# Kernel optimization log

Hardware: AMD Instinct MI355X
Metric: run time of the kernel (lower is better)

Reference implementation:

```python
import jax, jax.numpy as jnp
import numpy as np

HEADS = 8
DIM_HEAD = 160
QUERY_DIM = 1280
INNER = HEADS * DIM_HEAD  # 1280
B, S = 2, 4096


def setup_inputs() -> dict:
    key = jax.random.key(0)
    ks = jax.random.split(key, 7)
    scale = 0.02
    return {
        "hidden_states": jax.random.normal(ks[0], (B, QUERY_DIM, 1, S), jnp.float32),
        "context": jax.random.normal(ks[1], (B, QUERY_DIM, 1, S), jnp.float32),
        "mask": jnp.zeros((B, S, 1, 1), jnp.float32),
        "Wq": jax.random.normal(ks[2], (INNER, QUERY_DIM), jnp.float32) * scale,
        "Wk": jax.random.normal(ks[3], (INNER, QUERY_DIM), jnp.float32) * scale,
        "Wv": jax.random.normal(ks[4], (INNER, QUERY_DIM), jnp.float32) * scale,
        "Wout": jax.random.normal(ks[5], (QUERY_DIM, INNER), jnp.float32) * scale,
        "bout": jnp.zeros((QUERY_DIM,), jnp.float32),
    }


def reference(hidden_states, context, mask, Wq, Wk, Wv, Wout, bout):
    # hidden_states/context: [B, C, 1, S]; 1x1 conv == channel-dim matmul.
    x = hidden_states[:, :, 0, :]  # [B, C, Sq]
    c = context[:, :, 0, :]        # [B, C, Sk]
    scale = DIM_HEAD ** (-0.5)

    q = jnp.einsum("oc,bcs->bos", Wq, x)  # [B, inner, Sq]
    k = jnp.einsum("oc,bcs->bos", Wk, c)  # [B, inner, Sk]
    v = jnp.einsum("oc,bcs->bos", Wv, c)  # [B, inner, Sk]

    bsz, _, sq = q.shape
    sk = k.shape[-1]
    qh = q.reshape(bsz, HEADS, DIM_HEAD, sq)
    kh = k.reshape(bsz, HEADS, DIM_HEAD, sk)
    vh = v.reshape(bsz, HEADS, DIM_HEAD, sk)

    # split_einsum: per-head q^T k * scale, mask added per kv position,
    # softmax over kv dim. Vectorized over heads here (same math).
    scores = jnp.einsum("bhdq,bhdk->bhqk", qh, kh) * scale  # [B,H,Sq,Sk]
    scores = scores + mask[:, 0:, 0, 0][:, None, None, :]   # mask over kv
    weights = jax.nn.softmax(scores, axis=-1)
    attn = jnp.einsum("bhqk,bhdk->bhdq", weights, vh)       # [B,H,Dh,Sq]
    attn = attn.reshape(bsz, INNER, sq)

    out = jnp.einsum("oc,bcs->bos", Wout, attn) + bout[None, :, None]
    return out[:, :, None, :]  # [B, C, 1, Sq]
```

## Files before the change

### kernel.cpp

```cpp
#include <hip/hip_runtime.h>
#include <hip/hip_bf16.h>
#include <math.h>

#define B_   2
#define S_   4096
#define H_   8
#define D_   160
#define QD_  1280
#define SCALE 0.07905694150420949f
#define LOG2E 1.4426950408889634f

typedef unsigned short ushort_t;
typedef __attribute__((ext_vector_type(8))) short short8;
typedef __attribute__((ext_vector_type(4))) float f32x4;

#define MFMA16(a, b, c) __builtin_amdgcn_mfma_f32_16x16x32_bf16(a, b, c, 0, 0, 0)

__device__ __forceinline__ ushort_t f2bf(float f) {
  unsigned u = __float_as_uint(f);
  u += 0x7fffu + ((u >> 16) & 1u);
  return (ushort_t)(u >> 16);
}
__device__ __forceinline__ ushort_t f2bf_fast(float f) {
  return (ushort_t)((__float_as_uint(f) + 0x8000u) >> 16);
}

__device__ __forceinline__ void gload_lds16(const ushort_t* g, ushort_t* l) {
  __builtin_amdgcn_global_load_lds(
      (const __attribute__((address_space(1))) unsigned int*)(g),
      (__attribute__((address_space(3))) unsigned int*)(l), 16, 0, 0);
}

template <int CTRL>
__device__ __forceinline__ float dpp_mov(float x) {
  return __int_as_float(
      __builtin_amdgcn_update_dpp(0, __float_as_int(x), CTRL, 0xF, 0xF, true));
}
__device__ __forceinline__ float row_sum16(float x) {
  x += dpp_mov<0xB1>(x);
  x += dpp_mov<0x4E>(x);
  x += dpp_mov<0x124>(x);
  x += dpp_mov<0x128>(x);
  return x;
}

__global__ __launch_bounds__(256) void transpose_cvt2(
    const float* __restrict__ xs, const float* __restrict__ cs,
    ushort_t* __restrict__ Xt, ushort_t* __restrict__ Ct)
{
  const int z = blockIdx.z;
  const int b = z & 1;
  const float* src = (z < 2) ? xs : cs;
  ushort_t* dst    = (z < 2) ? Xt : Ct;
  const int s0 = blockIdx.x * 32;
  const int c0 = blockIdx.y * 32;
  __shared__ float T[32][33];
  const int t = threadIdx.x;
  const int sl = t & 31, cr = t >> 5;
#pragma unroll
  for (int i = 0; i < 4; ++i)
    T[cr + i * 8][sl] = src[((size_t)b * QD_ + c0 + cr + i * 8) * S_ + s0 + sl];
  __syncthreads();
  const int cl = (t & 7) * 4, sr = t >> 3;
  ushort4 v;
  v.x = f2bf(T[cl + 0][sr]);
  v.y = f2bf(T[cl + 1][sr]);
  v.z = f2bf(T[cl + 2][sr]);
  v.w = f2bf(T[cl + 3][sr]);
  *(ushort4*)(dst + ((size_t)b * S_ + s0 + sr) * QD_ + c0 + cl) = v;
}

__global__ __launch_bounds__(256) void cvt_w(
    const float* __restrict__ w0, const float* __restrict__ w1,
    const float* __restrict__ w2, const float* __restrict__ w3,
    ushort_t* __restrict__ o0, ushort_t* __restrict__ o1,
    ushort_t* __restrict__ o2, ushort_t* __restrict__ o3)
{
  const int which = blockIdx.y;
  const float* s = which == 0 ? w0 : which == 1 ? w1 : which == 2 ? w2 : w3;
  ushort_t* d    = which == 0 ? o0 : which == 1 ? o1 : which == 2 ? o2 : o3;
  const size_t i = ((size_t)blockIdx.x * 256 + threadIdx.x) * 4;
  const float4 f = *(const float4*)(s + i);
  ushort4 v;
  v.x = f2bf(f.x); v.y = f2bf(f.y); v.z = f2bf(f.z); v.w = f2bf(f.w);
  *(ushort4*)(d + i) = v;
}

#define GBM 128
#define GBN 128
#define GBK 32

#define GEMM_STAGE(tt, p, Abp, Bbp, Kv)                                        \
  {                                                                            \
    const int k0s = (tt) * GBK;                                                \
    _Pragma("unroll")                                                          \
    for (int i = 0; i < 2; ++i) {                                              \
      const int G = (i * 4 + wid) * 64 + lane;                                 \
      const int r = G >> 2, sl = G & 3;                                        \
      const int g = sl ^ (r & 3);                                              \
      gload_lds16(Abp + (size_t)(m0 + r) * (Kv) + k0s + g * 8,                 \
                  &As[p][(i * 4 + wid) * 512]);                                \
      gload_lds16(Bbp + (size_t)(n0 + r) * (Kv) + k0s + g * 8,                 \
                  &Bs[p][(i * 4 + wid) * 512]);                                \
    }                                                                          \
  }

__global__ __launch_bounds__(256) void gemm_qkv(
    const ushort_t* __restrict__ Xt, const ushort_t* __restrict__ Ct,
    const ushort_t* __restrict__ Wqb, const ushort_t* __restrict__ Wkb,
    const ushort_t* __restrict__ Wvb,
    ushort_t* __restrict__ q_ws, ushort_t* __restrict__ k_ws,
    ushort_t* __restrict__ v_ws)
{
  const size_t PB = (size_t)S_ * QD_;
  const int which = blockIdx.z >> 1, b = blockIdx.z & 1;
  const ushort_t* Ab;
  const ushort_t* Bb;
  ushort_t* Cb;
  int Nv, nx, cm, cn;
  if (which == 0) {
    Ab = Xt + (size_t)b * PB; Bb = Wqb; Cb = q_ws + (size_t)b * PB;
    Nv = QD_; nx = 10; cm = 4; cn = 10;
  } else if (which == 1) {
    Ab = Ct + (size_t)b * PB; Bb = Wkb; Cb = k_ws + (size_t)b * PB;
    Nv = QD_; nx = 10; cm = 4; cn = 10;
  } else {
    Ab = Wvb; Bb = Ct + (size_t)b * PB; Cb = v_ws + (size_t)b * PB;
    Nv = S_; nx = 32; cm = 5; cn = 8;
  }
  const int tiles_x = nx / cn;
  const int orig = blockIdx.x;
  const int xcd = orig & 7, idx = orig >> 3;
  const int trow = xcd / tiles_x, tcol = xcd - trow * tiles_x;
  const int m0 = (trow * cm + idx / cn) * GBM;
  const int n0 = (tcol * cn + idx % cn) * GBN;

  __shared__ ushort_t As[2][GBM * GBK];
  __shared__ ushort_t Bs[2][GBN * GBK];

  const int t = threadIdx.x;
  const int wid = t >> 6, lane = t & 63;
  const int l16 = lane & 15, quad = lane >> 4;
  const int wm = (wid >> 1) * 64, wn = (wid & 1) * 64;

  f32x4 acc[4][4];
#pragma unroll
  for (int i = 0; i < 4; ++i)
#pragma unroll
    for (int j = 0; j < 4; ++j) acc[i][j] = {0.f, 0.f, 0.f, 0.f};

  const int NIT = QD_ / GBK;
  GEMM_STAGE(0, 0, Ab, Bb, QD_);
  for (int it = 0; it < NIT; ++it) {
    asm volatile("s_waitcnt vmcnt(0)" ::: "memory");
    __builtin_amdgcn_sched_barrier(0);
    __builtin_amdgcn_s_barrier();
    __builtin_amdgcn_sched_barrier(0);
    if (it + 1 < NIT) {
      GEMM_STAGE(it + 1, (it + 1) & 1, Ab, Bb, QD_);
      __builtin_amdgcn_sched_barrier(0);
    }
    const int p = it & 1;
    short8 af[4], bfr[4];
#pragma unroll
    for (int mt = 0; mt < 4; ++mt) {
      const int r = wm + mt * 16 + l16;
      af[mt] = *(const short8*)&As[p][r * 32 + ((quad ^ (r & 3)) << 3)];
    }
#pragma unroll
    for (int nt = 0; nt < 4; ++nt) {
      const int r = wn + nt * 16 + l16;
      bfr[nt] = *(const short8*)&Bs[p][r * 32 + ((quad ^ (r & 3)) << 3)];
    }
#pragma unroll
    for (int mt = 0; mt < 4; ++mt)
#pragma unroll
      for (int nt = 0; nt < 4; ++nt)
        acc[mt][nt] = MFMA16(af[mt], bfr[nt], acc[mt][nt]);
  }

#pragma unroll
  for (int mt = 0; mt < 4; ++mt)
#pragma unroll
    for (int r = 0; r < 4; ++r) {
      const int row = m0 + wm + mt * 16 + quad * 4 + r;
      ushort_t* cr = Cb + (size_t)row * Nv + n0 + wn + l16;
#pragma unroll
      for (int nt = 0; nt < 4; ++nt) cr[nt * 16] = f2bf_fast(acc[mt][nt][r]);
    }
}

__global__ __launch_bounds__(256) void gemm_mfma(
    const ushort_t* __restrict__ A, const ushort_t* __restrict__ B,
    void* __restrict__ Cp, const float* __restrict__ bias,
    int M, int N, int K, int mode,
    size_t strideA, size_t strideB, size_t strideC,
    int cm, int cn)
{
  const int bz = blockIdx.z;
  const int nx = gridDim.x;
  const int tiles_x = nx / cn;
  const int orig = blockIdx.x + nx * blockIdx.y;
  const int xcd = orig & 7;
  const int idx = orig >> 3;
  const int trow = xcd / tiles_x, tcol = xcd - trow * tiles_x;
  const int m0 = (trow * cm + idx / cn) * GBM;
  const int n0 = (tcol * cn + idx % cn) * GBN;

  const ushort_t* __restrict__ Ab = A + (size_t)bz * strideA;
  const ushort_t* __restrict__ Bb = B + (size_t)bz * strideB;

  __shared__ ushort_t As[2][GBM * GBK];
  __shared__ ushort_t Bs[2][GBN * GBK];

  const int t = threadIdx.x;
  const int wid = t >> 6, lane = t & 63;
  const int l16 = lane & 15, quad = lane >> 4;
  const int wm = (wid >> 1) * 64, wn = (wid & 1) * 64;

  f32x4 acc[4][4];
#pragma unroll
  for (int i = 0; i < 4; ++i)
#pragma unroll
    for (int j = 0; j < 4; ++j) acc[i][j] = {0.f, 0.f, 0.f, 0.f};

  const int NIT = K / GBK;
  GEMM_STAGE(0, 0, Ab, Bb, K);
  for (int it = 0; it < NIT; ++it) {
    asm volatile("s_waitcnt vmcnt(0)" ::: "memory");
    __builtin_amdgcn_sched_barrier(0);
    __builtin_amdgcn_s_barrier();
    __builtin_amdgcn_sched_barrier(0);
    if (it + 1 < NIT) {
      GEMM_STAGE(it + 1, (it + 1) & 1, Ab, Bb, K);
      __builtin_amdgcn_sched_barrier(0);
    }
    const int p = it & 1;
    short8 af[4], bfr[4];
#pragma unroll
    for (int mt = 0; mt < 4; ++mt) {
      const int r = wm + mt * 16 + l16;
      af[mt] = *(const short8*)&As[p][r * 32 + ((quad ^ (r & 3)) << 3)];
    }
#pragma unroll
    for (int nt = 0; nt < 4; ++nt) {
      const int r = wn + nt * 16 + l16;
      bfr[nt] = *(const short8*)&Bs[p][r * 32 + ((quad ^ (r & 3)) << 3)];
    }
#pragma unroll
    for (int mt = 0; mt < 4; ++mt)
#pragma unroll
      for (int nt = 0; nt < 4; ++nt)
        acc[mt][nt] = MFMA16(af[mt], bfr[nt], acc[mt][nt]);
  }

  if (mode == 0) {
    ushort_t* C = (ushort_t*)Cp + (size_t)bz * strideC;
#pragma unroll
    for (int mt = 0; mt < 4; ++mt)
#pragma unroll
      for (int r = 0; r < 4; ++r) {
        const int row = m0 + wm + mt * 16 + quad * 4 + r;
        ushort_t* cr = C + (size_t)row * N + n0 + wn + l16;
#pragma unroll
        for (int nt = 0; nt < 4; ++nt) cr[nt * 16] = f2bf_fast(acc[mt][nt][r]);
      }
  } else {
    float* C = (float*)Cp + (size_t)bz * strideC;
#pragma unroll
    for (int mt = 0; mt < 4; ++mt)
#pragma unroll
      for (int r = 0; r < 4; ++r) {
        const int row = m0 + wm + mt * 16 + quad * 4 + r;
        const float bv = bias[row];
        float* cr = C + (size_t)row * N + n0 + wn + l16;
#pragma unroll
        for (int nt = 0; nt < 4; ++nt) cr[nt * 16] = acc[mt][nt][r] + bv;
      }
  }
}

#define TQ 128
#define TK 64
#define KTSTR 168
#define VTSTR 72
#define PSTR  72

__global__ __launch_bounds__(256, 2) void flash_attn_mfma(
    const ushort_t* __restrict__ qws, const ushort_t* __restrict__ kws,
    const ushort_t* __restrict__ vws, const float* __restrict__ mask,
    ushort_t* __restrict__ attn_out)
{
  const int b  = blockIdx.z;
  const int orig = blockIdx.x + 32 * blockIdx.y;
  const int swz  = ((orig & 7) << 5) | (orig >> 3);
  const int q0 = (swz & 31) * TQ;
  const int h  = swz >> 5;
  const int t  = threadIdx.x;
  const int wid  = t >> 6;
  const int lane = t & 63;
  const int l16  = lane & 15;
  const int quad = lane >> 4;

  __shared__ __align__(16) ushort_t smem[31744];
  ushort_t* Kt = smem;
  ushort_t* Vt = smem + 1344 * 8;
  ushort_t* Pp = smem + 2816 * 8;

  int goff[11];
#pragma unroll
  for (int jj = 0; jj < 11; ++jj) {
    const int j = jj * 4 + wid;
    const int slot = j * 64 + lane;
    int off;
    if (j < 21) {
      const int r = slot / 21, c = slot - r * 21;
      off = (c < 20) ? r * QD_ + c * 8 : 0;
    } else {
      const int vs = slot - 1344;
      const int r = vs / 9, c = vs - r * 9;
      off = (c < 8 && r < 160) ? r * S_ + c * 8 : 0;
    }
    goff[jj] = off;
  }

  const ushort_t* kg = kws + (size_t)b * S_ * QD_ + h * D_;
  const ushort_t* vg = vws + ((size_t)b * QD_ + h * D_) * S_;

  short8 aq[2][5];
#pragma unroll
  for (int mt = 0; mt < 2; ++mt) {
    const ushort_t* qrow =
        qws + ((size_t)(b * S_ + q0 + wid * 32 + mt * 16 + l16)) * QD_ + h * D_;
#pragma unroll
    for (int dc = 0; dc < 5; ++dc)
      aq[mt][dc] = *(const short8*)(qrow + dc * 32 + quad * 8);
  }

#pragma unroll
  for (int jj = 0; jj < 6; ++jj) {
    const int j = jj * 4 + wid;
    if (j < 21) gload_lds16(kg + goff[jj], &smem[(size_t)j * 512]);
  }
#pragma unroll
  for (int jj = 5; jj < 11; ++jj) {
    const int j = jj * 4 + wid;
    if (j >= 21) gload_lds16(vg + goff[jj], &smem[(size_t)j * 512]);
  }

  f32x4 Oa[2][10];
#pragma unroll
  for (int mt = 0; mt < 2; ++mt)
#pragma unroll
    for (int nt = 0; nt < 10; ++nt) Oa[mt][nt] = {0.f, 0.f, 0.f, 0.f};
  float lpart[2][4] = {{0.f, 0.f, 0.f, 0.f}, {0.f, 0.f, 0.f, 0.f}};
  const float SC2 = SCALE * LOG2E;

  const int pswz = quad << 4;
  const int prsw = (l16 >> 2) << 4;

  for (int kp0 = 0; kp0 < S_; kp0 += TK) {
    asm volatile("s_waitcnt vmcnt(5)" ::: "memory");
    __builtin_amdgcn_sched_barrier(0);
    __builtin_amdgcn_s_barrier();
    __builtin_amdgcn_sched_barrier(0);

    float mv[4];
#pragma unroll
    for (int c = 0; c < 4; ++c)
      mv[c] = mask[b * S_ + kp0 + c * 16 + l16] * LOG2E;

    f32x4 s[2][4];
#pragma unroll
    for (int mt = 0; mt < 2; ++mt)
#pragma unroll
      for (int c = 0; c < 4; ++c) s[mt][c] = {0.f, 0.f, 0.f, 0.f};
    __builtin_amdgcn_s_setprio(1);
#pragma unroll
    for (int dc = 0; dc < 5; ++dc) {
      short8 bb[4];
#pragma unroll
      for (int c = 0; c < 4; ++c)
        bb[c] = *(const short8*)&Kt[(c * 16 + l16) * KTSTR + dc * 32 + quad * 8];
#pragma unroll
      for (int mt = 0; mt < 2; ++mt)
#pragma unroll
        for (int c = 0; c < 4; ++c)
          s[mt][c] = MFMA16(aq[mt][dc], bb[c], s[mt][c]);
    }
    __builtin_amdgcn_s_setprio(0);

    ushort_t* pw = Pp + wid * (32 * PSTR);
#pragma unroll
    for (int mt = 0; mt < 2; ++mt)
#pragma unroll
      for (int r = 0; r < 4; ++r) {
        const float p0 = exp2f(s[mt][0][r] * SC2 + mv[0]);
        const float p1 = exp2f(s[mt][1][r] * SC2 + mv[1]);
        const float p2 = exp2f(s[mt][2][r] * SC2 + mv[2]);
        const float p3 = exp2f(s[mt][3][r] * SC2 + mv[3]);
        lpart[mt][r] += (p0 + p1) + (p2 + p3);
        ushort_t* prow = pw + (mt * 16 + quad * 4 + r) * PSTR;
        prow[(pswz ^  0) + l16] = f2bf_fast(p0);
        prow[(pswz ^ 16) + l16] = f2bf_fast(p1);
        prow[(pswz ^ 32) + l16] = f2bf_fast(p2);
        prow[(pswz ^ 48) + l16] = f2bf_fast(p3);
      }

    short8 ap[2][2];
#pragma unroll
    for (int mt = 0; mt < 2; ++mt) {
#pragma unroll
      for (int ks = 0; ks < 2; ++ks)
        ap[mt][ks] = *(const short8*)
            &Pp[wid * (32 * PSTR) + (mt * 16 + l16) * PSTR +
                ((ks * 32 + quad * 8) ^ prsw)];
    }

    __syncthreads();

    const int kn = kp0 + TK;
    if (kn < S_) {
      const ushort_t* kgn = kg + (size_t)kn * QD_;
#pragma unroll
      for (int jj = 0; jj < 6; ++jj) {
        const int j = jj * 4 + wid;
        if (j < 21) gload_lds16(kgn + goff[jj], &smem[(size_t)j * 512]);
      }
      __builtin_amdgcn_sched_barrier(0);
    }

    __builtin_amdgcn_s_setprio(1);
#pragma unroll
    for (int nt = 0; nt < 10; ++nt) {
      const short8 bv0 = *(const short8*)&Vt[(nt * 16 + l16) * VTSTR + quad * 8];
      const short8 bv1 = *(const short8*)&Vt[(nt * 16 + l16) * VTSTR + 32 + quad * 8];
#pragma unroll
      for (int mt = 0; mt < 2; ++mt) {
        Oa[mt][nt] = MFMA16(ap[mt][0], bv0, Oa[mt][nt]);
        Oa[mt][nt] = MFMA16(ap[mt][1], bv1, Oa[mt][nt]);
      }
    }
    __builtin_amdgcn_s_setprio(0);

    __builtin_amdgcn_sched_barrier(0);
    __builtin_amdgcn_s_barrier();
    __builtin_amdgcn_sched_barrier(0);

    if (kn < S_) {
      const ushort_t* vgn = vg + kn;
#pragma unroll
      for (int jj = 5; jj < 11; ++jj) {
        const int j = jj * 4 + wid;
        if (j >= 21) gload_lds16(vgn + goff[jj], &smem[(size_t)j * 512]);
      }
    }
  }

#pragma unroll
  for (int mt = 0; mt < 2; ++mt)
#pragma unroll
    for (int r = 0; r < 4; ++r) {
      const float l = row_sum16(lpart[mt][r]);
      const float inv = 1.f / l;
      const int qq = q0 + wid * 32 + mt * 16 + quad * 4 + r;
      ushort_t* orow = attn_out + ((size_t)(b * S_ + qq)) * QD_ + h * D_;
#pragma unroll
      for (int nt = 0; nt < 10; ++nt)
        orow[nt * 16 + l16] = f2bf_fast(Oa[mt][nt][r] * inv);
    }
}

extern "C" void kernel_launch(void* const* d_in, const int* in_sizes, int n_in,
                              void* d_out, int out_size, void* d_ws, size_t ws_size,
                              hipStream_t stream) {
  const float* x    = (const float*)d_in[0];
  const float* c    = (const float*)d_in[1];
  const float* mask = (const float*)d_in[2];
  const float* Wq   = (const float*)d_in[3];
  const float* Wk   = (const float*)d_in[4];
  const float* Wv   = (const float*)d_in[5];
  const float* Wout = (const float*)d_in[6];
  const float* bout = (const float*)d_in[7];
  float* out = (float*)d_out;

  const size_t PB   = (size_t)S_ * QD_;
  const size_t NELT = (size_t)B_ * PB;
  const size_t WN   = (size_t)QD_ * QD_;

  ushort_t* Xt    = (ushort_t*)d_ws;
  ushort_t* Ct    = Xt + NELT;
  ushort_t* Wqb   = Ct + NELT;
  ushort_t* Wkb   = Wqb + WN;
  ushort_t* Wvb   = Wkb + WN;
  ushort_t* Woutb = Wvb + WN;
  ushort_t* q_ws  = Woutb + WN;
  ushort_t* k_ws  = q_ws + NELT;
  ushort_t* v_ws  = k_ws + NELT;
  ushort_t* attn_ws = v_ws + NELT;

  const dim3 tgrid(S_ / 32, QD_ / 32, 2 * B_);
  transpose_cvt2<<<tgrid, 256, 0, stream>>>(x, c, Xt, Ct);
  cvt_w<<<dim3(WN / 1024, 4, 1), 256, 0, stream>>>(Wq, Wk, Wv, Wout,
                                                   Wqb, Wkb, Wvb, Woutb);

  gemm_qkv<<<dim3(320, 1, 6), 256, 0, stream>>>(Xt, Ct, Wqb, Wkb, Wvb,
                                                q_ws, k_ws, v_ws);

  const dim3 agrid(S_ / TQ, H_, B_);
  flash_attn_mfma<<<agrid, 256, 0, stream>>>(q_ws, k_ws, v_ws, mask, attn_ws);

  const dim3 gv(S_ / GBN, QD_ / GBM, B_);
  gemm_mfma<<<gv, 256, 0, stream>>>(Woutb, attn_ws, out, bout,
                                    QD_, S_, QD_, 1, 0, PB, PB, 5, 8);
}
```

Before: 540.9 us.

## Triple-buffer GEMM LDS stages with two tiles of loads in flight

Both GEMM kernels move from double to triple buffering in LDS and prefetch two K-tiles ahead. The wait becomes vmcnt(4) instead of vmcnt(0), so the next tile's global-to-LDS loads can stay outstanding while the current tile is consumed. This is meant to hide more global memory latency in the projection GEMMs. In exchange LDS use rises by half, which may lower occupancy, and correctness now depends on each stage issuing exactly four loads per thread.

Result: faster. 525.4 us (-2.9%).

```diff
diff --git a/kernel.cpp b/kernel.cpp
--- a/kernel.cpp
+++ b/kernel.cpp
@@ -103,6 +103,39 @@
       gload_lds16(Bbp + (size_t)(n0 + r) * (Kv) + k0s + g * 8,                 \
                   &Bs[p][(i * 4 + wid) * 512]);                                \
     }                                                                          \
+  }
+
+#define GEMM_PIPE_ITER(it, NIT, Abp, Bbp, Kv)                                  \
+  {                                                                            \
+    if ((it) + 1 < (NIT)) {                                                    \
+      asm volatile("s_waitcnt vmcnt(4)" ::: "memory");                         \
+    } else {                                                                   \
+      asm volatile("s_waitcnt vmcnt(0)" ::: "memory");                         \
+    }                                                                          \
+    __builtin_amdgcn_sched_barrier(0);                                         \
+    __builtin_amdgcn_s_barrier();                                              \
+    __builtin_amdgcn_sched_barrier(0);                                         \
+    if ((it) + 2 < (NIT)) {                                                    \
+      GEMM_STAGE((it) + 2, ((it) + 2) % 3, Abp, Bbp, Kv);                      \
+      __builtin_amdgcn_sched_barrier(0);                                       \
+    }                                                                          \
+    const int p = (it) % 3;                                                    \
+    short8 af[4], bfr[4];                                                      \
+    _Pragma("unroll")                                                          \
+    for (int mt = 0; mt < 4; ++mt) {                                           \
+      const int r = wm + mt * 16 + l16;                                        \
+      af[mt] = *(const short8*)&As[p][r * 32 + ((quad ^ (r & 3)) << 3)];       \
+    }                                                                          \
+    _Pragma("unroll")                                                          \
+    for (int nt = 0; nt < 4; ++nt) {                                           \
+      const int r = wn + nt * 16 + l16;                                        \
+      bfr[nt] = *(const short8*)&Bs[p][r * 32 + ((quad ^ (r & 3)) << 3)];      \
+    }                                                                          \
+    _Pragma("unroll")                                                          \
+    for (int mt = 0; mt < 4; ++mt)                                             \
+      _Pragma("unroll")                                                        \
+      for (int nt = 0; nt < 4; ++nt)                                           \
+        acc[mt][nt] = MFMA16(af[mt], bfr[nt], acc[mt][nt]);                    \
   }
 
 __global__ __launch_bounds__(256) void gemm_qkv(
@@ -135,8 +168,8 @@
   const int m0 = (trow * cm + idx / cn) * GBM;
   const int n0 = (tcol * cn + idx % cn) * GBN;
 
-  __shared__ ushort_t As[2][GBM * GBK];
-  __shared__ ushort_t Bs[2][GBN * GBK];
+  __shared__ ushort_t As[3][GBM * GBK];
+  __shared__ ushort_t Bs[3][GBN * GBK];
 
   const int t = threadIdx.x;
   const int wid = t >> 6, lane = t & 63;
@@ -151,32 +184,9 @@
 
   const int NIT = QD_ / GBK;
   GEMM_STAGE(0, 0, Ab, Bb, QD_);
+  GEMM_STAGE(1, 1, Ab, Bb, QD_);
   for (int it = 0; it < NIT; ++it) {
-    asm volatile("s_waitcnt vmcnt(0)" ::: "memory");
-    __builtin_amdgcn_sched_barrier(0);
-    __builtin_amdgcn_s_barrier();
-    __builtin_amdgcn_sched_barrier(0);
-    if (it + 1 < NIT) {
-      GEMM_STAGE(it + 1, (it + 1) & 1, Ab, Bb, QD_);
-      __builtin_amdgcn_sched_barrier(0);
-    }
-    const int p = it & 1;
-    short8 af[4], bfr[4];
-#pragma unroll
-    for (int mt = 0; mt < 4; ++mt) {
-      const int r = wm + mt * 16 + l16;
-      af[mt] = *(const short8*)&As[p][r * 32 + ((quad ^ (r & 3)) << 3)];
-    }
-#pragma unroll
-    for (int nt = 0; nt < 4; ++nt) {
-      const int r = wn + nt * 16 + l16;
-      bfr[nt] = *(const short8*)&Bs[p][r * 32 + ((quad ^ (r & 3)) << 3)];
-    }
-#pragma unroll
-    for (int mt = 0; mt < 4; ++mt)
-#pragma unroll
-      for (int nt = 0; nt < 4; ++nt)
-        acc[mt][nt] = MFMA16(af[mt], bfr[nt], acc[mt][nt]);
+    GEMM_PIPE_ITER(it, NIT, Ab, Bb, QD_);
   }
 
 #pragma unroll
@@ -210,8 +220,8 @@
   const ushort_t* __restrict__ Ab = A + (size_t)bz * strideA;
   const ushort_t* __restrict__ Bb = B + (size_t)bz * strideB;
 
-  __shared__ ushort_t As[2][GBM * GBK];
-  __shared__ ushort_t Bs[2][GBN * GBK];
+  __shared__ ushort_t As[3][GBM * GBK];
+  __shared__ ushort_t Bs[3][GBN * GBK];
 
   const int t = threadIdx.x;
   const int wid = t >> 6, lane = t & 63;
@@ -226,32 +236,9 @@
 
   const int NIT = K / GBK;
   GEMM_STAGE(0, 0, Ab, Bb, K);
+  GEMM_STAGE(1, 1, Ab, Bb, K);
   for (int it = 0; it < NIT; ++it) {
-    asm volatile("s_waitcnt vmcnt(0)" ::: "memory");
-    __builtin_amdgcn_sched_barrier(0);
-    __builtin_amdgcn_s_barrier();
-    __builtin_amdgcn_sched_barrier(0);
-    if (it + 1 < NIT) {
-      GEMM_STAGE(it + 1, (it + 1) & 1, Ab, Bb, K);
-      __builtin_amdgcn_sched_barrier(0);
-    }
-    const int p = it & 1;
-    short8 af[4], bfr[4];
-#pragma unroll
-    for (int mt = 0; mt < 4; ++mt) {
-      const int r = wm + mt * 16 + l16;
-      af[mt] = *(const short8*)&As[p][r * 32 + ((quad ^ (r & 3)) << 3)];
-    }
-#pragma unroll
-    for (int nt = 0; nt < 4; ++nt) {
-      const int r = wn + nt * 16 + l16;
-      bfr[nt] = *(const short8*)&Bs[p][r * 32 + ((quad ^ (r & 3)) << 3)];
-    }
-#pragma unroll
-    for (int mt = 0; mt < 4; ++mt)
-#pragma unroll
-      for (int nt = 0; nt < 4; ++nt)
-        acc[mt][nt] = MFMA16(af[mt], bfr[nt], acc[mt][nt]);
+    GEMM_PIPE_ITER(it, NIT, Ab, Bb, K);
   }
 
   if (mode == 0) {
```
